# Kernel tuning notes

Measured on AMD Instinct MI355X. Metric: run time of the kernel, lower is better.

Reference implementation:

```python
import jax, jax.numpy as jnp
import numpy as np

N_HEAD = 16
HEAD_SIZE = 64

def setup_inputs() -> dict:
    key = jax.random.key(0)
    ks = jax.random.split(key, 5)
    B, T, C = 2, 2048, 1024
    s = 0.02
    return {
        "x": jax.random.normal(ks[0], (B, T, C), dtype=jnp.float32),
        "We": jax.random.normal(ks[1], (3 * C, C), dtype=jnp.float32) * s,
        "be": jax.random.normal(ks[2], (3 * C,), dtype=jnp.float32) * s,
        "Wp": jax.random.normal(ks[3], (C, C), dtype=jnp.float32) * s,
        "bp": jax.random.normal(ks[4], (C,), dtype=jnp.float32) * s,
    }

def reference(x, We, be, Wp, bp):
    B, T, C = x.shape
    H, D = N_HEAD, HEAD_SIZE
    qkv = x @ We.T + be                      # [B,T,3C]
    q, k, v = jnp.split(qkv, 3, axis=-1)
    # [B,H,T,D]
    q = q.reshape(B, T, H, D).transpose(0, 2, 1, 3)
    k = k.reshape(B, T, H, D).transpose(0, 2, 1, 3)
    v = v.reshape(B, T, H, D).transpose(0, 2, 1, 3)
    scale = 1.0 / jnp.sqrt(jnp.asarray(D, dtype=x.dtype))
    att = jnp.einsum('bhqd,bhkd->bhqk', q, k) * scale
    causal = jnp.tril(jnp.ones((T, T), dtype=bool))
    att = jnp.where(causal, att, -jnp.inf)
    att = jax.nn.softmax(att, axis=-1)
    y = jnp.einsum('bhqk,bhkd->bhqd', att, v)   # [B,H,T,D]
    y = y.transpose(0, 2, 1, 3).reshape(B, T, C)
    return y @ Wp.T + bp
```

## Files before the change

kernel.cpp:

```cpp
#include <hip/hip_runtime.h>
#include <hip/hip_bf16.h>
#include <stdint.h>
#include <stddef.h>

typedef short s8v __attribute__((ext_vector_type(8)));
typedef float f4v __attribute__((ext_vector_type(4)));

__device__ inline float b2f(short s) {
    union { unsigned u; float f; } x;
    x.u = ((unsigned)(unsigned short)s) << 16;
    return x.f;
}
__device__ inline short f2b(float f) {
    union { float f; unsigned u; } x;
    x.f = f;
    unsigned r = x.u + 0x7FFF + ((x.u >> 16) & 1);
    return (short)(r >> 16);
}

__device__ __forceinline__ void gl16(const short* g, short* l) {
    __builtin_amdgcn_global_load_lds(
        (const __attribute__((address_space(1))) void*)g,
        (__attribute__((address_space(3))) void*)l,
        16, 0, 0);
}

__global__ __launch_bounds__(256) void convert_bf16(
    const void* s0, short* d0, size_t c0,
    const void* s1, short* d1, size_t c1,
    const void* s2, short* d2, size_t c2,
    const void* s3, short* d3, size_t c3,
    const void* s4, short* d4, size_t c4,
    int* __restrict__ flagout)
{
    int hit = 0;
    const unsigned* xw = (const unsigned*)s0;
    for (int i = threadIdx.x & 63; i < 1024; i += 64) {
        unsigned e = ((xw[i] & 0xFFFFu) >> 7) & 0xFFu;
        if (e >= 0x8Au) hit = 1;
    }
    const bool f32 = (__ballot(hit != 0) != 0ull);
    if (blockIdx.x == 0 && threadIdx.x == 0) *flagout = f32 ? 1 : 0;

    const void* srcs[5] = {s0, s1, s2, s3, s4};
    short* dsts[5] = {d0, d1, d2, d3, d4};
    size_t cnts[5] = {c0, c1, c2, c3, c4};
    size_t total = c0 + c1 + c2 + c3 + c4;
    size_t stride = (size_t)gridDim.x * blockDim.x;
    for (size_t c = (size_t)blockIdx.x * blockDim.x + threadIdx.x; c < total; c += stride) {
        size_t r = c; int s = 0;
        while (r >= cnts[s]) { r -= cnts[s]; s++; }
        short* d = dsts[s] + r * 8;
        if (f32) {
            const float* p = (const float*)srcs[s] + r * 8;
            f4v a = *(const f4v*)p;
            f4v b = *(const f4v*)(p + 4);
            s8v v;
            v[0] = f2b(a[0]); v[1] = f2b(a[1]); v[2] = f2b(a[2]); v[3] = f2b(a[3]);
            v[4] = f2b(b[0]); v[5] = f2b(b[1]); v[6] = f2b(b[2]); v[7] = f2b(b[3]);
            *(s8v*)d = v;
        } else {
            *(s8v*)d = *(const s8v*)((const short*)srcs[s] + r * 8);
        }
    }
}

#define BKK 64

template<int QKV, int TBM, int TBN, int MINW>
__global__ __launch_bounds__(256, MINW) void gemm_bt_bias(
    const short* __restrict__ A,
    const short* __restrict__ B,
    const short* __restrict__ bias,
    void* __restrict__ C,
    short* __restrict__ vT,
    int M, int N, int K, int ldc,
    const int* __restrict__ flagp, int oDyn)
{
    const bool of32 = oDyn && (*flagp != 0);
    const int MT = TBM / 32, NT = TBN / 32;

    __shared__ __align__(16) short smem[(TBM + TBN) * BKK];
    short* sA = smem;
    short* sB = smem + TBM * BKK;

    const int tid  = threadIdx.x;
    const int lane = tid & 63;
    const int w    = tid >> 6;
    const int wm   = (w >> 1) * (TBM / 2);
    const int wn   = (w & 1) * (TBN / 2);
    const int quad = lane >> 4;
    const int l16  = lane & 15;

    const int bid0 = blockIdx.y * (int)gridDim.x + blockIdx.x;
    const int nwg  = (int)(gridDim.x * gridDim.y);
    const int lb   = (bid0 & 7) * (nwg >> 3) + (bid0 >> 3);
    const int m0 = (lb / (int)gridDim.x) * TBM;
    const int n0 = (lb % (int)gridDim.x) * TBN;

    f4v acc[MT][NT];
    const f4v vzero = {0.0f, 0.0f, 0.0f, 0.0f};
#pragma unroll
    for (int i = 0; i < MT; i++)
#pragma unroll
        for (int j = 0; j < NT; j++) acc[i][j] = vzero;

    const int ACH = TBM * 8;
    for (int k0 = 0; k0 < K; k0 += BKK) {
        __syncthreads();
#pragma unroll
        for (int i = 0; i < (TBM + TBN) / 32; i++) {
            int c  = i * 256 + tid;
            int cb = i * 256 + (tid & 192);
            if (c < ACH) {
                int r = c >> 3, kk = (c & 7) * 8;
                gl16(A + (size_t)(m0 + r) * K + k0 + kk, sA + cb * 8);
            } else {
                int c2 = c - ACH, cb2 = cb - ACH;
                int r = c2 >> 3, kk = (c2 & 7) * 8;
                gl16(B + (size_t)(n0 + r) * K + k0 + kk, sB + cb2 * 8);
            }
        }
        __syncthreads();
#pragma unroll
        for (int s = 0; s < 2; s++) {
            s8v af[MT], bf[NT];
#pragma unroll
            for (int t = 0; t < MT; t++)
                af[t] = *(const s8v*)(sA + (wm + t * 16 + l16) * BKK + s * 32 + quad * 8);
#pragma unroll
            for (int t = 0; t < NT; t++)
                bf[t] = *(const s8v*)(sB + (wn + t * 16 + l16) * BKK + s * 32 + quad * 8);
#pragma unroll
            for (int mt = 0; mt < MT; mt++)
#pragma unroll
                for (int nt = 0; nt < NT; nt++)
                    acc[mt][nt] = __builtin_amdgcn_mfma_f32_16x16x32_bf16(
                        af[mt], bf[nt], acc[mt][nt], 0, 0, 0);
        }
    }

    if (QKV && n0 >= 2048) {
        static_assert(!QKV || (TBM == 128 && TBN == 128), "V transpose assumes 128x128");
        const int bq = m0 >> 11;
#pragma unroll
        for (int hm = 0; hm < 2; hm++) {
            __syncthreads();
            if ((w >> 1) == hm) {
#pragma unroll
                for (int nt = 0; nt < NT; nt++) {
                    int nl = wn + nt * 16 + l16;
                    float bv = b2f(bias[n0 + nl]);
#pragma unroll
                    for (int mt = 0; mt < MT; mt++)
#pragma unroll
                        for (int r = 0; r < 4; r++) {
                            int ml2 = mt * 16 + quad * 4 + r;
                            smem[nl * 72 + ml2] = f2b(acc[mt][nt][r] + bv);
                        }
                }
            }
            __syncthreads();
#pragma unroll
            for (int i = 0; i < 4; i++) {
                int c = i * 256 + tid;
                int nl = c >> 3, col = (c & 7) * 8;
                int nn = n0 + nl;
                int hh = (nn - 2048) >> 6, d = nn & 63;
                short* dst = vT + (((size_t)(bq * 16 + hh)) * 64 + d) * 2048
                           + (m0 & 2047) + hm * 64 + col;
                *(s8v*)dst = *(const s8v*)(smem + nl * 72 + col);
            }
        }
    } else if (QKV) {
        const float osc = (n0 < 1024) ? 0.125f : 1.0f;
#pragma unroll
        for (int hm = 0; hm < 2; hm++) {
            __syncthreads();
            if ((w >> 1) == hm) {
#pragma unroll
                for (int nt = 0; nt < NT; nt++) {
                    int nl = wn + nt * 16 + l16;
                    float bv = b2f(bias[n0 + nl]);
#pragma unroll
                    for (int mt = 0; mt < MT; mt++)
#pragma unroll
                        for (int r = 0; r < 4; r++) {
                            int ml2 = mt * 16 + quad * 4 + r;
                            smem[ml2 * 144 + nl] = f2b((acc[mt][nt][r] + bv) * osc);
                        }
                }
            }
            __syncthreads();
#pragma unroll
            for (int i = 0; i < 4; i++) {
                int c = i * 256 + tid;
                int m = c >> 4, ncol = (c & 15) * 8;
                *(s8v*)((short*)C + (size_t)(m0 + hm * 64 + m) * ldc + n0 + ncol) =
                    *(const s8v*)(smem + m * 144 + ncol);
            }
        }
    } else {
#pragma unroll
        for (int nt = 0; nt < NT; nt++) {
            int n = n0 + wn + nt * 16 + l16;
            float bv = b2f(bias[n]);
#pragma unroll
            for (int mt = 0; mt < MT; mt++) {
#pragma unroll
                for (int r = 0; r < 4; r++) {
                    int m = m0 + wm + mt * 16 + quad * 4 + r;
                    float v = acc[mt][nt][r] + bv;
                    if (of32) ((float*)C)[(size_t)m * ldc + n] = v;
                    else      ((short*)C)[(size_t)m * ldc + n] = f2b(v);
                }
            }
        }
    }
}

#define LP 72

template<int PARTS>
__global__ __launch_bounds__(256) void attn_flash(
    const short* __restrict__ qk,
    const short* __restrict__ vt,
    short* __restrict__ y,
    short* __restrict__ Opart,
    float* __restrict__ Lpart)
{
    const int T = 2048, LDQ = 2048;
    __shared__ __align__(16) short sK[64 * LP];
    __shared__ __align__(16) short sVT[64 * LP];
    __shared__ __align__(16) short sP[4][16 * LP];

    const int tid  = threadIdx.x;
    const int lane = tid & 63;
    const int w    = tid >> 6;
    const int quad = lane >> 4;
    const int l16  = lane & 15;

    int part, qt, bh, u;
    if (PARTS == 2) {
        part = blockIdx.x & 1;
        int rest = blockIdx.x >> 1;
        qt = 31 - (rest >> 5);
        bh = rest & 31;
        u  = bh * 32 + qt;
    } else {
        part = 0;
        qt = 31 - (blockIdx.x >> 5);
        bh = blockIdx.x & 31;
        u  = 0;
    }
    const int b = bh >> 4;
    const int h = bh & 15;

    const int n    = qt + 1;
    const int half = (n + 1) >> 1;
    const int klo  = (PARTS == 2 && part) ? half : 0;
    const int khi  = (PARTS == 2 && !part) ? half : n;

    if (PARTS == 2 && klo >= khi) {
        s8v z;
#pragma unroll
        for (int j = 0; j < 8; j++) z[j] = 0;
        s8v* ob = (s8v*)(Opart + ((size_t)(part * 1024 + u)) * 4096);
        for (int i = tid; i < 512; i += 256) ob[i] = z;
        if (tid < 64) Lpart[(size_t)(part * 1024 + u) * 64 + tid] = 0.0f;
        return;
    }

    const size_t qkbase = (size_t)b * T * LDQ;
    const short* Kbase  = qk + qkbase + 1024 + h * 64;
    const short* Vbase  = vt + (size_t)bh * 64 * 2048;

    s8v qf[2];
    {
        int qrow = qt * 64 + w * 16 + l16;
        const short* qp = qk + qkbase + (size_t)qrow * LDQ + h * 64 + quad * 8;
        qf[0] = *(const s8v*)(qp);
        qf[1] = *(const s8v*)(qp + 32);
    }

    const int r0 = tid >> 3;
    const int dd = (tid & 7) * 8;

    const f4v vzero = {0.0f, 0.0f, 0.0f, 0.0f};
    f4v o[4];
#pragma unroll
    for (int i = 0; i < 4; i++) o[i] = vzero;
    float lsum[4] = {0.0f, 0.0f, 0.0f, 0.0f};

    s8v ka0, ka1, va0, va1, kb0, kb1, vb0, vb1;
    ka0 = *(const s8v*)(Kbase + (size_t)(klo * 64 + r0) * LDQ + dd);
    ka1 = *(const s8v*)(Kbase + (size_t)(klo * 64 + r0 + 32) * LDQ + dd);
    va0 = *(const s8v*)(Vbase + (size_t)r0 * 2048 + klo * 64 + dd);
    va1 = *(const s8v*)(Vbase + (size_t)(r0 + 32) * 2048 + klo * 64 + dd);
    if (klo + 1 < khi) {
        kb0 = *(const s8v*)(Kbase + (size_t)((klo + 1) * 64 + r0) * LDQ + dd);
        kb1 = *(const s8v*)(Kbase + (size_t)((klo + 1) * 64 + r0 + 32) * LDQ + dd);
        vb0 = *(const s8v*)(Vbase + (size_t)r0 * 2048 + (klo + 1) * 64 + dd);
        vb1 = *(const s8v*)(Vbase + (size_t)(r0 + 32) * 2048 + (klo + 1) * 64 + dd);
    }

    auto body = [&](s8v& kr0, s8v& kr1, s8v& vv0, s8v& vv1, int kt) {
        __syncthreads();
        *(s8v*)(sK  + r0 * LP + dd)        = kr0;
        *(s8v*)(sK  + (r0 + 32) * LP + dd) = kr1;
        *(s8v*)(sVT + r0 * LP + dd)        = vv0;
        *(s8v*)(sVT + (r0 + 32) * LP + dd) = vv1;
        if (kt + 2 < khi) {
            kr0 = *(const s8v*)(Kbase + (size_t)((kt + 2) * 64 + r0) * LDQ + dd);
            kr1 = *(const s8v*)(Kbase + (size_t)((kt + 2) * 64 + r0 + 32) * LDQ + dd);
            vv0 = *(const s8v*)(Vbase + (size_t)r0 * 2048 + (kt + 2) * 64 + dd);
            vv1 = *(const s8v*)(Vbase + (size_t)(r0 + 32) * 2048 + (kt + 2) * 64 + dd);
        }
        __syncthreads();

        f4v sacc[4];
#pragma unroll
        for (int nt = 0; nt < 4; nt++) {
            sacc[nt] = vzero;
            s8v kf0 = *(const s8v*)(sK + (nt * 16 + l16) * LP + quad * 8);
            s8v kf1 = *(const s8v*)(sK + (nt * 16 + l16) * LP + 32 + quad * 8);
            sacc[nt] = __builtin_amdgcn_mfma_f32_16x16x32_bf16(qf[0], kf0, sacc[nt], 0, 0, 0);
            sacc[nt] = __builtin_amdgcn_mfma_f32_16x16x32_bf16(qf[1], kf1, sacc[nt], 0, 0, 0);
        }

        short* pp = sP[w];
        const bool diag = (kt == qt);
#pragma unroll
        for (int nt = 0; nt < 4; nt++) {
#pragma unroll
            for (int r = 0; r < 4; r++) {
                float p = __expf(sacc[nt][r]);
                if (diag) {
                    int q = w * 16 + quad * 4 + r;
                    int k = nt * 16 + l16;
                    if (k > q) p = 0.0f;
                }
                union { float f; unsigned u; } c2; c2.f = p;
                short p16 = (short)(c2.u >> 16);
                c2.u &= 0xFFFF0000u;
                lsum[r] += c2.f;
                pp[(quad * 4 + r) * LP + nt * 16 + l16] = p16;
            }
        }

        s8v pf0 = *(const s8v*)(pp + l16 * LP + quad * 8);
        s8v pf1 = *(const s8v*)(pp + l16 * LP + 32 + quad * 8);
#pragma unroll
        for (int dt = 0; dt < 4; dt++) {
            s8v vf0 = *(const s8v*)(sVT + (dt * 16 + l16) * LP + quad * 8);
            s8v vf1 = *(const s8v*)(sVT + (dt * 16 + l16) * LP + 32 + quad * 8);
            o[dt] = __builtin_amdgcn_mfma_f32_16x16x32_bf16(pf0, vf0, o[dt], 0, 0, 0);
            o[dt] = __builtin_amdgcn_mfma_f32_16x16x32_bf16(pf1, vf1, o[dt], 0, 0, 0);
        }
    };

    for (int kt = klo; kt < khi; kt += 2) {
        body(ka0, ka1, va0, va1, kt);
        if (kt + 1 < khi)
            body(kb0, kb1, vb0, vb1, kt + 1);
    }

#pragma unroll
    for (int r = 0; r < 4; r++) {
        float s = lsum[r];
        s += __shfl_xor(s, 1, 64);
        s += __shfl_xor(s, 2, 64);
        s += __shfl_xor(s, 4, 64);
        s += __shfl_xor(s, 8, 64);
        lsum[r] = s;
    }

    if (PARTS == 2) {
        short* ob = Opart + ((size_t)(part * 1024 + u)) * 4096;
#pragma unroll
        for (int dt = 0; dt < 4; dt++)
#pragma unroll
            for (int r = 0; r < 4; r++)
                ob[(w * 16 + quad * 4 + r) * 64 + dt * 16 + l16] = f2b(o[dt][r]);
        if (l16 == 0) {
#pragma unroll
            for (int r = 0; r < 4; r++)
                Lpart[(size_t)(part * 1024 + u) * 64 + w * 16 + quad * 4 + r] = lsum[r];
        }
    } else {
#pragma unroll
        for (int r = 0; r < 4; r++) lsum[r] = 1.0f / lsum[r];
#pragma unroll
        for (int dt = 0; dt < 4; dt++)
#pragma unroll
            for (int r = 0; r < 4; r++) {
                int qrow = qt * 64 + w * 16 + quad * 4 + r;
                int d = dt * 16 + l16;
                y[((size_t)b * T + qrow) * 1024 + h * 64 + d] = f2b(o[dt][r] * lsum[r]);
            }
    }
}

__global__ __launch_bounds__(256) void attn_combine(
    const short* __restrict__ Opart,
    const float* __restrict__ Lpart,
    short* __restrict__ y)
{
    const int u  = blockIdx.x;
    const int bh = u >> 5, qt = u & 31;
    const int b = bh >> 4, h = bh & 15;
    const int t = threadIdx.x;
    const int q = t >> 2, dg = (t & 3) * 16;

    float l = Lpart[(size_t)u * 64 + q] + Lpart[(size_t)(1024 + u) * 64 + q];
    float rl = 1.0f / l;
    const short* p0 = Opart + (size_t)u * 4096 + q * 64 + dg;
    const short* p1 = Opart + (size_t)(1024 + u) * 4096 + q * 64 + dg;
    short* yo = y + ((size_t)b * 2048 + qt * 64 + q) * 1024 + h * 64 + dg;
#pragma unroll
    for (int hv = 0; hv < 2; hv++) {
        s8v a = *(const s8v*)(p0 + hv * 8);
        s8v c = *(const s8v*)(p1 + hv * 8);
        s8v r;
#pragma unroll
        for (int j = 0; j < 8; j++) r[j] = f2b((b2f(a[j]) + b2f(c[j])) * rl);
        *(s8v*)(yo + hv * 8) = r;
    }
}

extern "C" void kernel_launch(void* const* d_in, const int* in_sizes, int n_in,
                              void* d_out, int out_size, void* d_ws, size_t ws_size,
                              hipStream_t stream)
{
    char* p = (char*)d_ws;
    int*   flag = (int*)p;                 p += 16;
    short* qk   = (short*)p;               p += (size_t)4096 * 2048 * 2;
    short* vT   = (short*)p;               p += (size_t)32 * 64 * 2048 * 2;
    short* xb   = (short*)p;               p += (size_t)4096 * 1024 * 2;
    short* Web  = (short*)p;               p += (size_t)3072 * 1024 * 2;
    short* Wpb  = (short*)p;               p += (size_t)1024 * 1024 * 2;
    short* beb  = (short*)p;               p += 3072 * 2;
    short* bpb  = (short*)p;               p += 1024 * 2;
    short* Opart = (short*)p;              p += (size_t)2 * 1024 * 4096 * 2;
    float* Lpart = (float*)p;              p += (size_t)2 * 1024 * 64 * 4;
    short* y = xb;
    const size_t need = (size_t)(p - (char*)d_ws);
    const bool split = (ws_size >= need);

    convert_bf16<<<dim3(4098), 256, 0, stream>>>(
        d_in[0], xb,  (size_t)4096 * 1024 / 8,
        d_in[1], Web, (size_t)3072 * 1024 / 8,
        d_in[2], beb, (size_t)3072 / 8,
        d_in[3], Wpb, (size_t)1024 * 1024 / 8,
        d_in[4], bpb, (size_t)1024 / 8,
        flag);

    gemm_bt_bias<1, 128, 128, 3><<<dim3(3072 / 128, 4096 / 128), 256, 0, stream>>>(
        xb, Web, beb, qk, vT, 4096, 3072, 1024, 2048, flag, 0);

    if (split) {
        attn_flash<2><<<dim3(2048), 256, 0, stream>>>(qk, vT, nullptr, Opart, Lpart);
        attn_combine<<<dim3(1024), 256, 0, stream>>>(Opart, Lpart, y);
    } else {
        attn_flash<1><<<dim3(1024), 256, 0, stream>>>(qk, vT, y, nullptr, nullptr);
    }

    gemm_bt_bias<0, 128, 64, 2><<<dim3(1024 / 64, 4096 / 128), 256, 0, stream>>>(
        y, Wpb, bpb, d_out, nullptr, 4096, 1024, 1024, 1024, flag, 1);
}
```

Before: 190.0 us.

## Fuse split-K attention combine into flash kernel via atomic last-block ticket

Removes the separate attn_combine launch. Each split attention block writes its partial O and L, increments a per-tile atomic counter, and whichever block arrives second does the combine for that tile. The counters are zeroed inside the conversion kernel. This saves one kernel launch and gives better tail overlap, at the cost of extra threadfences and atomics, plus a dependency on counter reset and memory ordering being correct.

```diff
diff --git a/kernel.cpp b/kernel.cpp
--- a/kernel.cpp
+++ b/kernel.cpp
@@ -31,7 +31,7 @@
     const void* s2, short* d2, size_t c2,
     const void* s3, short* d3, size_t c3,
     const void* s4, short* d4, size_t c4,
-    int* __restrict__ flagout)
+    int* __restrict__ flagout, int* __restrict__ cntz)
 {
     int hit = 0;
     const unsigned* xw = (const unsigned*)s0;
@@ -41,6 +41,9 @@
     }
     const bool f32 = (__ballot(hit != 0) != 0ull);
     if (blockIdx.x == 0 && threadIdx.x == 0) *flagout = f32 ? 1 : 0;
+    if (cntz && blockIdx.x == 1) {
+        for (int i = threadIdx.x; i < 1024; i += 256) cntz[i] = 0;
+    }
 
     const void* srcs[5] = {s0, s1, s2, s3, s4};
     short* dsts[5] = {d0, d1, d2, d3, d4};
@@ -219,6 +222,27 @@
     }
 }
 
+__device__ __forceinline__ void combine_u(
+    const short* __restrict__ Opart, const float* __restrict__ Lpart,
+    short* __restrict__ y, int u, int b, int h, int qt, int tid)
+{
+    const int q = tid >> 2, dg = (tid & 3) * 16;
+    float l = Lpart[(size_t)u * 64 + q] + Lpart[(size_t)(1024 + u) * 64 + q];
+    float rl = 1.0f / l;
+    const short* p0 = Opart + (size_t)u * 4096 + q * 64 + dg;
+    const short* p1 = Opart + (size_t)(1024 + u) * 4096 + q * 64 + dg;
+    short* yo = y + ((size_t)b * 2048 + qt * 64 + q) * 1024 + h * 64 + dg;
+#pragma unroll
+    for (int hv = 0; hv < 2; hv++) {
+        s8v a = *(const s8v*)(p0 + hv * 8);
+        s8v c = *(const s8v*)(p1 + hv * 8);
+        s8v r;
+#pragma unroll
+        for (int j = 0; j < 8; j++) r[j] = f2b((b2f(a[j]) + b2f(c[j])) * rl);
+        *(s8v*)(yo + hv * 8) = r;
+    }
+}
+
 #define LP 72
 
 template<int PARTS>
@@ -227,12 +251,14 @@
     const short* __restrict__ vt,
     short* __restrict__ y,
     short* __restrict__ Opart,
-    float* __restrict__ Lpart)
+    float* __restrict__ Lpart,
+    int* __restrict__ cnt)
 {
     const int T = 2048, LDQ = 2048;
     __shared__ __align__(16) short sK[64 * LP];
     __shared__ __align__(16) short sVT[64 * LP];
     __shared__ __align__(16) short sP[4][16 * LP];
+    __shared__ int sTicket;
 
     const int tid  = threadIdx.x;
     const int lane = tid & 63;
@@ -268,6 +294,13 @@
         s8v* ob = (s8v*)(Opart + ((size_t)(part * 1024 + u)) * 4096);
         for (int i = tid; i < 512; i += 256) ob[i] = z;
         if (tid < 64) Lpart[(size_t)(part * 1024 + u) * 64 + tid] = 0.0f;
+        __threadfence();
+        if (tid == 0) sTicket = atomicAdd(&cnt[u], 1);
+        __syncthreads();
+        if (sTicket == 1) {
+            __threadfence();
+            combine_u(Opart, Lpart, y, u, b, h, qt, tid);
+        }
         return;
     }
 
@@ -387,6 +420,13 @@
             for (int r = 0; r < 4; r++)
                 Lpart[(size_t)(part * 1024 + u) * 64 + w * 16 + quad * 4 + r] = lsum[r];
         }
+        __threadfence();
+        if (tid == 0) sTicket = atomicAdd(&cnt[u], 1);
+        __syncthreads();
+        if (sTicket == 1) {
+            __threadfence();
+            combine_u(Opart, Lpart, y, u, b, h, qt, tid);
+        }
     } else {
 #pragma unroll
         for (int r = 0; r < 4; r++) lsum[r] = 1.0f / lsum[r];
@@ -398,33 +438,6 @@
                 int d = dt * 16 + l16;
                 y[((size_t)b * T + qrow) * 1024 + h * 64 + d] = f2b(o[dt][r] * lsum[r]);
             }
-    }
-}
-
-__global__ __launch_bounds__(256) void attn_combine(
-    const short* __restrict__ Opart,
-    const float* __restrict__ Lpart,
-    short* __restrict__ y)
-{
-    const int u  = blockIdx.x;
-    const int bh = u >> 5, qt = u & 31;
-    const int b = bh >> 4, h = bh & 15;
-    const int t = threadIdx.x;
-    const int q = t >> 2, dg = (t & 3) * 16;
-
-    float l = Lpart[(size_t)u * 64 + q] + Lpart[(size_t)(1024 + u) * 64 + q];
-    float rl = 1.0f / l;
-    const short* p0 = Opart + (size_t)u * 4096 + q * 64 + dg;
-    const short* p1 = Opart + (size_t)(1024 + u) * 4096 + q * 64 + dg;
-    short* yo = y + ((size_t)b * 2048 + qt * 64 + q) * 1024 + h * 64 + dg;
-#pragma unroll
-    for (int hv = 0; hv < 2; hv++) {
-        s8v a = *(const s8v*)(p0 + hv * 8);
-        s8v c = *(const s8v*)(p1 + hv * 8);
-        s8v r;
-#pragma unroll
-        for (int j = 0; j < 8; j++) r[j] = f2b((b2f(a[j]) + b2f(c[j])) * rl);
-        *(s8v*)(yo + hv * 8) = r;
     }
 }
 
@@ -443,6 +456,7 @@
     short* bpb  = (short*)p;               p += 1024 * 2;
     short* Opart = (short*)p;              p += (size_t)2 * 1024 * 4096 * 2;
     float* Lpart = (float*)p;              p += (size_t)2 * 1024 * 64 * 4;
+    int*   cnt   = (int*)p;                p += 1024 * 4;
     short* y = xb;
     const size_t need = (size_t)(p - (char*)d_ws);
     const bool split = (ws_size >= need);
@@ -453,16 +467,15 @@
         d_in[2], beb, (size_t)3072 / 8,
         d_in[3], Wpb, (size_t)1024 * 1024 / 8,
         d_in[4], bpb, (size_t)1024 / 8,
-        flag);
+        flag, split ? cnt : nullptr);
 
     gemm_bt_bias<1, 128, 128, 3><<<dim3(3072 / 128, 4096 / 128), 256, 0, stream>>>(
         xb, Web, beb, qk, vT, 4096, 3072, 1024, 2048, flag, 0);
 
     if (split) {
-        attn_flash<2><<<dim3(2048), 256, 0, stream>>>(qk, vT, nullptr, Opart, Lpart);
-        attn_combine<<<dim3(1024), 256, 0, stream>>>(Opart, Lpart, y);
+        attn_flash<2><<<dim3(2048), 256, 0, stream>>>(qk, vT, y, Opart, Lpart, cnt);
     } else {
-        attn_flash<1><<<dim3(1024), 256, 0, stream>>>(qk, vT, y, nullptr, nullptr);
+        attn_flash<1><<<dim3(1024), 256, 0, stream>>>(qk, vT, y, nullptr, nullptr, nullptr);
     }
 
     gemm_bt_bias<0, 128, 64, 2><<<dim3(1024 / 64, 4096 / 128), 256, 0, stream>>>(
```

After: 674.2 us. 3.55x slower.
